# Kernel tuning notes

Hardware: AMD Instinct MI355X
Metric: run time of the kernel (lower is better)

## Reference

```python
import jax, jax.numpy as jnp
import numpy as np


@jax.custom_vjp
def sign_ste(x):
    return jnp.sign(x)

def _sign_fwd(x):
    return jnp.sign(x), x

def _sign_bwd(x, g):
    # straight-through estimator: pass grad where |x| <= 1
    return (g * (jnp.abs(x) <= 1.0).astype(g.dtype),)

sign_ste.defvjp(_sign_fwd, _sign_bwd)


def setup_inputs() -> dict:
    key = jax.random.key(0)
    ks = jax.random.split(key, 4)
    B = 262144
    return {
        "x": jax.random.normal(ks[0], (B, 256), dtype=jnp.float32),
        "w1": jax.random.normal(ks[1], (128, 256), dtype=jnp.float32) * 0.1,
        "b1": jnp.zeros((128,), dtype=jnp.float32),
        "w2": jax.random.normal(ks[2], (64, 128), dtype=jnp.float32) * 0.1,
        "b2": jnp.zeros((64,), dtype=jnp.float32),
        "w3": jax.random.normal(ks[3], (1, 64), dtype=jnp.float32) * 0.1,
        "b3": jnp.zeros((1,), dtype=jnp.float32),
    }


def reference(x, w1, b1, w2, b2, w3, b3):
    # x: [B, 256]; binarized XNOR-style 3-layer MLP, training path (sigmoid out)
    h = sign_ste(x)
    h = sign_ste(h @ sign_ste(w1).T + b1)   # [B, 128]
    h = sign_ste(h @ sign_ste(w2).T + b2)   # [B, 64]
    out = h @ sign_ste(w3).T + b3            # [B, 1]
    return jax.nn.sigmoid(out)
```

## Files before the change

kernel.cpp:

```cpp
#include <hip/hip_runtime.h>
#include <stdint.h>

typedef unsigned long long u64;


__global__ __launch_bounds__(256) void pack_weights(
    const float* __restrict__ w1, const float* __restrict__ w2,
    const float* __restrict__ w3, u64* __restrict__ wp)
{
    int t = blockIdx.x * blockDim.x + threadIdx.x;
    if (t < 512) {
        int r = t >> 2, j = t & 3;
        const float* src = w1 + r * 256 + j;
        u64 word = 0;
        #pragma unroll
        for (int l = 0; l < 64; ++l)
            word |= (u64)(src[l * 4] < 0.0f) << l;
        wp[t] = word;
    } else if (t < 640) {
        int idx = t - 512;
        int r = idx >> 1, j = idx & 1;
        const float* src = w2 + r * 128 + j * 64;
        u64 word = 0;
        #pragma unroll
        for (int l = 0; l < 64; ++l)
            word |= (u64)(src[l] < 0.0f) << l;
        wp[t] = word;
    } else if (t == 640) {
        u64 word = 0;
        #pragma unroll
        for (int l = 0; l < 64; ++l)
            word |= (u64)(w3[l] < 0.0f) << l;
        wp[t] = word;
    }
}

__global__ __launch_bounds__(256) void xnor_fwd(
    const float* __restrict__ x,
    const float* __restrict__ b1, const float* __restrict__ b2,
    const float* __restrict__ b3,
    const u64* __restrict__ w1p, const u64* __restrict__ w2p,
    const u64* __restrict__ w3p,
    float* __restrict__ out, int B)
{
    const int lane = threadIdx.x & 63;
    const int wib  = threadIdx.x >> 6;
    const int wpb  = blockDim.x >> 6;
    const int g    = blockIdx.x * wpb + wib;
    const int nwav = gridDim.x * wpb;

    u64 w1a[4], w1b[4], w2r[2];
    #pragma unroll
    for (int j = 0; j < 4; ++j) {
        w1a[j] = w1p[lane * 4 + j];
        w1b[j] = w1p[(lane + 64) * 4 + j];
    }
    w2r[0] = w2p[lane * 2 + 0];
    w2r[1] = w2p[lane * 2 + 1];
    const u64 w3w = w3p[0];
    const float b1a = b1[lane], b1b = b1[lane + 64];
    const float b2v = b2[lane];
    const float b3v = b3[0];

    const int rpw = B / nwav;
    int row = g * rpw;
    const char* xb = (const char*)x;
    unsigned off = (unsigned)row * 1024u + ((unsigned)lane << 4);

    for (int it = 0; it < rpw; ++it, ++row, off += 1024u) {
        const float4 xv = *reinterpret_cast<const float4*>(xb + off);

        const u64 sx0 = __ballot(xv.x < 0.0f);
        const u64 sx1 = __ballot(xv.y < 0.0f);
        const u64 sx2 = __ballot(xv.z < 0.0f);
        const u64 sx3 = __ballot(xv.w < 0.0f);

        const float prod = xv.x * xv.y * xv.z * xv.w;
        const u64 zb = __ballot(prod == 0.0f);

        int pa, pb, nzx;
        if (zb == 0ull) {
            nzx = 256;
            pa = __popcll(sx0 ^ w1a[0]) + __popcll(sx1 ^ w1a[1])
               + __popcll(sx2 ^ w1a[2]) + __popcll(sx3 ^ w1a[3]);
            pb = __popcll(sx0 ^ w1b[0]) + __popcll(sx1 ^ w1b[1])
               + __popcll(sx2 ^ w1b[2]) + __popcll(sx3 ^ w1b[3]);
        } else {
            const u64 mx0 = __ballot(xv.x != 0.0f);
            const u64 mx1 = __ballot(xv.y != 0.0f);
            const u64 mx2 = __ballot(xv.z != 0.0f);
            const u64 mx3 = __ballot(xv.w != 0.0f);
            nzx = __popcll(mx0) + __popcll(mx1) + __popcll(mx2) + __popcll(mx3);
            pa = __popcll((sx0 ^ w1a[0]) & mx0) + __popcll((sx1 ^ w1a[1]) & mx1)
               + __popcll((sx2 ^ w1a[2]) & mx2) + __popcll((sx3 ^ w1a[3]) & mx3);
            pb = __popcll((sx0 ^ w1b[0]) & mx0) + __popcll((sx1 ^ w1b[1]) & mx1)
               + __popcll((sx2 ^ w1b[2]) & mx2) + __popcll((sx3 ^ w1b[3]) & mx3);
        }

        const float ta = (float)(nzx - 2 * pa) + b1a;
        const float tb = (float)(nzx - 2 * pb) + b1b;

        const u64 s1_0 = __ballot(ta < 0.0f);
        const u64 s1_1 = __ballot(tb < 0.0f);
        const u64 m1_0 = __ballot(ta != 0.0f);
        const u64 m1_1 = __ballot(tb != 0.0f);
        const int nz1 = __popcll(m1_0) + __popcll(m1_1);

        const int p2 = __popcll((s1_0 ^ w2r[0]) & m1_0)
                     + __popcll((s1_1 ^ w2r[1]) & m1_1);
        const float t2 = (float)(nz1 - 2 * p2) + b2v;

        const u64 s2 = __ballot(t2 < 0.0f);
        const u64 m2 = __ballot(t2 != 0.0f);
        const int nz2 = __popcll(m2);

        const int p3 = __popcll((s2 ^ w3w) & m2);
        const float t3 = (float)(nz2 - 2 * p3) + b3v;
        const float res = 1.0f / (1.0f + __expf(-t3));
        if (lane == 0) out[row] = res;
    }

    const int rem_base = nwav * rpw;
    const int trow = rem_base + g;
    if (trow < B) {
        const float4 xv = *reinterpret_cast<const float4*>(
            xb + (unsigned)trow * 1024u + ((unsigned)lane << 4));
        const u64 sx0 = __ballot(xv.x < 0.0f);
        const u64 sx1 = __ballot(xv.y < 0.0f);
        const u64 sx2 = __ballot(xv.z < 0.0f);
        const u64 sx3 = __ballot(xv.w < 0.0f);
        const u64 mx0 = __ballot(xv.x != 0.0f);
        const u64 mx1 = __ballot(xv.y != 0.0f);
        const u64 mx2 = __ballot(xv.z != 0.0f);
        const u64 mx3 = __ballot(xv.w != 0.0f);
        const int nzx = __popcll(mx0) + __popcll(mx1) + __popcll(mx2) + __popcll(mx3);
        const int pa = __popcll((sx0 ^ w1a[0]) & mx0) + __popcll((sx1 ^ w1a[1]) & mx1)
                     + __popcll((sx2 ^ w1a[2]) & mx2) + __popcll((sx3 ^ w1a[3]) & mx3);
        const int pb = __popcll((sx0 ^ w1b[0]) & mx0) + __popcll((sx1 ^ w1b[1]) & mx1)
                     + __popcll((sx2 ^ w1b[2]) & mx2) + __popcll((sx3 ^ w1b[3]) & mx3);
        const float ta = (float)(nzx - 2 * pa) + b1a;
        const float tb = (float)(nzx - 2 * pb) + b1b;
        const u64 s1_0 = __ballot(ta < 0.0f);
        const u64 s1_1 = __ballot(tb < 0.0f);
        const u64 m1_0 = __ballot(ta != 0.0f);
        const u64 m1_1 = __ballot(tb != 0.0f);
        const int nz1 = __popcll(m1_0) + __popcll(m1_1);
        const int p2 = __popcll((s1_0 ^ w2r[0]) & m1_0)
                     + __popcll((s1_1 ^ w2r[1]) & m1_1);
        const float t2 = (float)(nz1 - 2 * p2) + b2v;
        const u64 s2 = __ballot(t2 < 0.0f);
        const u64 m2 = __ballot(t2 != 0.0f);
        const int nz2 = __popcll(m2);
        const int p3 = __popcll((s2 ^ w3w) & m2);
        const float t3 = (float)(nz2 - 2 * p3) + b3v;
        const float res = 1.0f / (1.0f + __expf(-t3));
        if (lane == 0) out[trow] = res;
    }
}

extern "C" void kernel_launch(void* const* d_in, const int* in_sizes, int n_in,
                              void* d_out, int out_size, void* d_ws, size_t ws_size,
                              hipStream_t stream)
{
    const float* x  = (const float*)d_in[0];
    const float* w1 = (const float*)d_in[1];
    const float* b1 = (const float*)d_in[2];
    const float* w2 = (const float*)d_in[3];
    const float* b2 = (const float*)d_in[4];
    const float* w3 = (const float*)d_in[5];
    const float* b3 = (const float*)d_in[6];
    float* out = (float*)d_out;
    const int B = in_sizes[0] / 256;

    u64* wp = (u64*)d_ws;

    pack_weights<<<3, 256, 0, stream>>>(w1, w2, w3, wp);

    const int blocks = 2048;
    xnor_fwd<<<blocks, 256, 0, stream>>>(x, b1, b2, b3,
                                         wp, wp + 512, wp + 640, out, B);
}
```

Before: 56.59 us.

## Grid-stride row assignment, unroll loop, fold biases into comparisons

Rows are now assigned to waves in a grid-stride pattern, so concurrent wavefronts read adjacent 1KB rows, instead of each wave walking a contiguous chunk. The loop is unrolled by two and the no-zero branch is marked likely. Bias adds are replaced by comparisons against precomputed negated biases. The intent is better DRAM locality and more loads in flight for this bandwidth-bound kernel, at the cost of a different address pattern and some register pressure from the unroll.

```diff
diff --git a/kernel.cpp b/kernel.cpp
--- a/kernel.cpp
+++ b/kernel.cpp
@@ -58,16 +58,18 @@
     w2r[0] = w2p[lane * 2 + 0];
     w2r[1] = w2p[lane * 2 + 1];
     const u64 w3w = w3p[0];
-    const float b1a = b1[lane], b1b = b1[lane + 64];
-    const float b2v = b2[lane];
-    const float b3v = b3[0];
+    const float nb1a = -b1[lane], nb1b = -b1[lane + 64];
+    const float nb2v = -b2[lane];
+    const float b3v  = b3[0];
 
-    const int rpw = B / nwav;
-    int row = g * rpw;
+    const int iters = B / nwav;
+    const unsigned stride = (unsigned)nwav << 10;
+    unsigned off = ((unsigned)g << 10) + ((unsigned)lane << 4);
     const char* xb = (const char*)x;
-    unsigned off = (unsigned)row * 1024u + ((unsigned)lane << 4);
+    int row = g;
 
-    for (int it = 0; it < rpw; ++it, ++row, off += 1024u) {
+    #pragma unroll 2
+    for (int it = 0; it < iters; ++it, row += nwav, off += stride) {
         const float4 xv = *reinterpret_cast<const float4*>(xb + off);
 
         const u64 sx0 = __ballot(xv.x < 0.0f);
@@ -79,7 +81,7 @@
         const u64 zb = __ballot(prod == 0.0f);
 
         int pa, pb, nzx;
-        if (zb == 0ull) {
+        if (__builtin_expect(zb == 0ull, 1)) {
             nzx = 256;
             pa = __popcll(sx0 ^ w1a[0]) + __popcll(sx1 ^ w1a[1])
                + __popcll(sx2 ^ w1a[2]) + __popcll(sx3 ^ w1a[3]);
@@ -97,21 +99,21 @@
                + __popcll((sx2 ^ w1b[2]) & mx2) + __popcll((sx3 ^ w1b[3]) & mx3);
         }
 
-        const float ta = (float)(nzx - 2 * pa) + b1a;
-        const float tb = (float)(nzx - 2 * pb) + b1b;
+        const float fa = (float)(nzx - 2 * pa);
+        const float fb = (float)(nzx - 2 * pb);
 
-        const u64 s1_0 = __ballot(ta < 0.0f);
-        const u64 s1_1 = __ballot(tb < 0.0f);
-        const u64 m1_0 = __ballot(ta != 0.0f);
-        const u64 m1_1 = __ballot(tb != 0.0f);
+        const u64 s1_0 = __ballot(fa < nb1a);
+        const u64 s1_1 = __ballot(fb < nb1b);
+        const u64 m1_0 = __ballot(fa != nb1a);
+        const u64 m1_1 = __ballot(fb != nb1b);
         const int nz1 = __popcll(m1_0) + __popcll(m1_1);
 
         const int p2 = __popcll((s1_0 ^ w2r[0]) & m1_0)
                      + __popcll((s1_1 ^ w2r[1]) & m1_1);
-        const float t2 = (float)(nz1 - 2 * p2) + b2v;
+        const float fc = (float)(nz1 - 2 * p2);
 
-        const u64 s2 = __ballot(t2 < 0.0f);
-        const u64 m2 = __ballot(t2 != 0.0f);
+        const u64 s2 = __ballot(fc < nb2v);
+        const u64 m2 = __ballot(fc != nb2v);
         const int nz2 = __popcll(m2);
 
         const int p3 = __popcll((s2 ^ w3w) & m2);
@@ -120,8 +122,7 @@
         if (lane == 0) out[row] = res;
     }
 
-    const int rem_base = nwav * rpw;
-    const int trow = rem_base + g;
+    const int trow = iters * nwav + g;
     if (trow < B) {
         const float4 xv = *reinterpret_cast<const float4*>(
             xb + (unsigned)trow * 1024u + ((unsigned)lane << 4));
@@ -138,18 +139,18 @@
                      + __popcll((sx2 ^ w1a[2]) & mx2) + __popcll((sx3 ^ w1a[3]) & mx3);
         const int pb = __popcll((sx0 ^ w1b[0]) & mx0) + __popcll((sx1 ^ w1b[1]) & mx1)
                      + __popcll((sx2 ^ w1b[2]) & mx2) + __popcll((sx3 ^ w1b[3]) & mx3);
-        const float ta = (float)(nzx - 2 * pa) + b1a;
-        const float tb = (float)(nzx - 2 * pb) + b1b;
-        const u64 s1_0 = __ballot(ta < 0.0f);
-        const u64 s1_1 = __ballot(tb < 0.0f);
-        const u64 m1_0 = __ballot(ta != 0.0f);
-        const u64 m1_1 = __ballot(tb != 0.0f);
+        const float fa = (float)(nzx - 2 * pa);
+        const float fb = (float)(nzx - 2 * pb);
+        const u64 s1_0 = __ballot(fa < nb1a);
+        const u64 s1_1 = __ballot(fb < nb1b);
+        const u64 m1_0 = __ballot(fa != nb1a);
+        const u64 m1_1 = __ballot(fb != nb1b);
         const int nz1 = __popcll(m1_0) + __popcll(m1_1);
         const int p2 = __popcll((s1_0 ^ w2r[0]) & m1_0)
                      + __popcll((s1_1 ^ w2r[1]) & m1_1);
-        const float t2 = (float)(nz1 - 2 * p2) + b2v;
-        const u64 s2 = __ballot(t2 < 0.0f);
-        const u64 m2 = __ballot(t2 != 0.0f);
+        const float fc = (float)(nz1 - 2 * p2);
+        const u64 s2 = __ballot(fc < nb2v);
+        const u64 m2 = __ballot(fc != nb2v);
         const int nz2 = __popcll(m2);
         const int p3 = __popcll((s2 ^ w3w) & m2);
         const float t3 = (float)(nz2 - 2 * p3) + b3v;
```

Result: faster. 54.44 us (-3.8%).
